# Kernel tuning notes

Hardware: AMD Instinct MI355X
Metric: run time of the kernel (lower is better)

Reference implementation:

```python
import jax, jax.numpy as jnp
import numpy as np

B, K, N, DIM, C_IN = 4, 2048, 4096, 3, 61
IN = DIM + C_IN        # 64, deepset input size
H1, H2 = 128, 128      # neighbor_xf hidden sizes
OUT = 64               # c_out // heads
HEADS = 4
EPS = 1e-5             # BatchNorm eps


def _lin(key, i, o):
    return jax.random.normal(key, (i, o), jnp.float32) * (1.0 / np.sqrt(i))


def setup_inputs() -> dict:
    key = jax.random.key(0)
    ks = jax.random.split(key, 12)
    return {
        "keys": jax.random.normal(ks[0], (B, K, DIM), jnp.float32),
        "points": jax.random.normal(ks[1], (B, N, DIM), jnp.float32),
        "feats": jax.random.normal(ks[2], (B, N, C_IN), jnp.float32),
        "nx_w1": _lin(ks[3], IN, H1), "nx_b1": jnp.zeros((H1,), jnp.float32),
        "nx_w2": _lin(ks[4], H1, H2), "nx_b2": jnp.zeros((H2,), jnp.float32),
        "nx_w3": _lin(ks[5], H2, OUT), "nx_b3": jnp.zeros((OUT,), jnp.float32),
        "sx_w1": _lin(ks[6], IN, IN), "sx_b1": jnp.zeros((IN,), jnp.float32),
        "sx_w2": _lin(ks[7], IN, IN), "sx_b2": jnp.zeros((IN,), jnp.float32),
        "sx_w3": _lin(ks[8], IN, IN), "sx_b3": jnp.zeros((IN,), jnp.float32),
        "att_w": _lin(ks[9], 2 * IN, HEADS * IN),
        "att_b": jnp.zeros((HEADS * IN,), jnp.float32),
        "att_q": jax.random.normal(ks[10], (HEADS, IN), jnp.float32) * 0.1,
        "bn_gamma": jnp.ones((IN,), jnp.float32),
        "bn_beta": jnp.zeros((IN,), jnp.float32),
        "neighbors": 32,
    }


def _mlp3(x, w1, b1, w2, b2, w3, b3):
    # per-element deepset MLP: Linear-ReLU-Linear-ReLU-Linear
    h = jax.nn.relu(x @ w1 + b1)
    h = jax.nn.relu(h @ w2 + b2)
    return h @ w3 + b3


def _forward(keys, points, feats, nx_w1, nx_b1, nx_w2, nx_b2, nx_w3, nx_b3,
             sx_w1, sx_b1, sx_w2, sx_b2, sx_w3, sx_b3,
             att_w, att_b, att_q, bn_gamma, bn_beta, neighbors):
    b = keys.shape[0]
    # Euclidean dist_fn: dist_vec [B,K,N,dim], dist [B,K,N], all points valid
    rel = points[:, None, :, :] - keys[:, :, None, :]
    dist = jnp.sqrt(jnp.sum(rel * rel, axis=-1))
    _, idx = jax.lax.top_k(-dist, neighbors)                   # [B,K,k] nearest
    nrel = jnp.take_along_axis(rel, idx[..., None], axis=2)    # [B,K,k,dim]
    bidx = jnp.arange(b)[:, None, None]
    nfeat = feats[bidx, idx]                                   # [B,K,k,c_in]
    comb = jnp.concatenate([nrel, nfeat], axis=-1)             # [B,K,k,in]
    lat = _mlp3(comb, nx_w1, nx_b1, nx_w2, nx_b2, nx_w3, nx_b3)  # [B,K,k,out]
    # BatchNorm1d (training-mode batch stats) over flattened [B*K*k, in]
    flat = comb.reshape(-1, comb.shape[-1])
    mean = jnp.mean(flat, axis=0)
    var = jnp.var(flat, axis=0)
    norm = (comb - mean) * jax.lax.rsqrt(var + EPS) * bn_gamma + bn_beta
    # SelfAttention: deepset sum-pooled context + per-neighbor softmax weights
    set_feat = jnp.sum(_mlp3(norm, sx_w1, sx_b1, sx_w2, sx_b2, sx_w3, sx_b3), axis=2)
    comb_feat = jnp.concatenate(
        [norm, jnp.broadcast_to(set_feat[:, :, None, :], norm.shape)], axis=-1)
    heads = (comb_feat @ att_w + att_b).reshape(comb_feat.shape[:3] + (HEADS, -1))
    e = jnp.sum(heads * att_q, axis=-1)                        # [B,K,k,H]
    w = jax.nn.softmax(e, axis=-2)                             # softmax over neighbor axis
    out = jnp.einsum('bkno,bknh->bkoh', lat, w)                # weighted reduce over k
    return out.reshape(out.shape[:2] + (-1,))                  # [B,K,out*H]


def reference(keys, points, feats, nx_w1, nx_b1, nx_w2, nx_b2, nx_w3, nx_b3,
              sx_w1, sx_b1, sx_w2, sx_b2, sx_w3, sx_b3,
              att_w, att_b, att_q, bn_gamma, bn_beta, neighbors):
    return _forward(keys, points, feats, nx_w1, nx_b1, nx_w2, nx_b2, nx_w3, nx_b3,
                    sx_w1, sx_b1, sx_w2, sx_b2, sx_w3, sx_b3,
                    att_w, att_b, att_q, bn_gamma, bn_beta, neighbors)
```

## Files before the change

### kernel.cpp

```cpp
#include <hip/hip_runtime.h>
#include <math.h>

#define BATCH 4
#define KQ    2048
#define NPTS  4096
#define CIN   61
#define KNN   32
#define ROWS  (BATCH*KQ*KNN)

#define OFF_IDX  0
#define OFF_ACC  524288
#define OFF_ATTA 557056
#define OFF_W1F  558080
#define OFF_W2F  574464
#define OFF_W3F  607232

typedef __attribute__((ext_vector_type(8)))  short bfrag;
typedef __attribute__((ext_vector_type(4)))  unsigned ufrag;
typedef __attribute__((ext_vector_type(16))) float cfrag;

__device__ __forceinline__ unsigned short bf16_rne(float x) {
  unsigned u = __float_as_uint(x);
  unsigned r = u + 0x7fffu + ((u >> 16) & 1u);
  return (unsigned short)(r >> 16);
}
__device__ __forceinline__ float4 ld4u(const float* p) {
  float4 r; __builtin_memcpy(&r, p, 16); return r;
}
__device__ __forceinline__ unsigned cvtpk(float lo, float hi) {
  unsigned r;
  asm("v_cvt_pk_bf16_f32 %0, %1, %2" : "=v"(r) : "v"(lo), "v"(hi));
  return r;
}
__device__ __forceinline__ float up_lo(unsigned pk) { return __uint_as_float(pk << 16); }
__device__ __forceinline__ float up_hi(unsigned pk) { return __uint_as_float(pk & 0xffff0000u); }

__device__ __forceinline__ cfrag zero16() {
  cfrag z;
#pragma unroll
  for (int i = 0; i < 16; ++i) z[i] = 0.f;
  return z;
}
__device__ __forceinline__ cfrag mfma_bu(bfrag a, ufrag b, cfrag c) {
  return __builtin_amdgcn_mfma_f32_32x32x16_bf16(a, __builtin_bit_cast(bfrag, b), c, 0, 0, 0);
}
__device__ __forceinline__ cfrag mfma_ub(ufrag a, bfrag b, cfrag c) {
  return __builtin_amdgcn_mfma_f32_32x32x16_bf16(__builtin_bit_cast(bfrag, a), b, c, 0, 0, 0);
}
__device__ __forceinline__ cfrag mfma_uu(ufrag a, ufrag b, cfrag c) {
  return __builtin_amdgcn_mfma_f32_32x32x16_bf16(__builtin_bit_cast(bfrag, a), __builtin_bit_cast(bfrag, b), c, 0, 0, 0);
}

#define NCAND 128

template<int NS>
__device__ __forceinline__ void select_emit(
    const unsigned* __restrict__ VAL, const unsigned short* __restrict__ IDXL,
    int mcount, unsigned hib, unsigned lob, int lane,
    const float* __restrict__ Pb, float kx, float ky, float kz,
    unsigned short* __restrict__ dst, int* __restrict__ SEL,
    float* __restrict__ accs) {
  const unsigned long long lmask = (1ull << lane) - 1ull;
  unsigned e[NS];
#pragma unroll
  for (int s = 0; s < NS; ++s) {
    int ei = s*64 + lane;
    e[s] = (ei < mcount) ? VAL[ei] : 0xffffffffu;
  }
  unsigned lo2 = lob, hi2 = hib;
  while (lo2 < hi2) {
    unsigned mid = lo2 + ((hi2 - lo2) >> 1);
    int c = 0;
#pragma unroll
    for (int s = 0; s < NS; ++s) c += (int)__popcll(__ballot(e[s] <= mid));
    if (c == KNN) { hi2 = mid; break; }
    if (c > KNN) hi2 = mid; else lo2 = mid + 1;
  }
  const unsigned T = hi2;
  float r0=0.f,r1=0.f,r2=0.f,r3=0.f,r4=0.f,r5=0.f;
  int base2 = 0;
#pragma unroll
  for (int s = 0; s < NS; ++s) {
    bool p = (e[s] <= T);
    unsigned long long m = __ballot(p);
    if (p) {
      int pos = base2 + (int)__popcll(m & lmask);
      if (pos < KNN) {
        int n = (int)IDXL[s*64 + lane];
        SEL[pos] = n;
        dst[pos] = (unsigned short)n;
        float dx = Pb[n*3+0]-kx, dy = Pb[n*3+1]-ky, dz = Pb[n*3+2]-kz;
        r0 += dx; r1 += dy; r2 += dz;
        r3 += dx*dx; r4 += dy*dy; r5 += dz*dz;
      }
    }
    base2 += (int)__popcll(m);
  }
#pragma unroll
  for (int off = 32; off > 0; off >>= 1) {
    r0 += __shfl_down(r0, off); r1 += __shfl_down(r1, off);
    r2 += __shfl_down(r2, off); r3 += __shfl_down(r3, off);
    r4 += __shfl_down(r4, off); r5 += __shfl_down(r5, off);
  }
  if (lane == 0) {
    atomicAdd(&accs[0], r0); atomicAdd(&accs[1], r1); atomicAdd(&accs[2], r2);
    atomicAdd(&accs[64], r3); atomicAdd(&accs[65], r4); atomicAdd(&accs[66], r5);
  }
}

__global__ __launch_bounds__(256, 4) void topk_kernel(
    const float* __restrict__ keys, const float* __restrict__ points,
    const float* __restrict__ feats,
    const float* __restrict__ w1, const float* __restrict__ w2,
    const float* __restrict__ w3,
    const float* __restrict__ att_w, const float* __restrict__ att_q,
    unsigned short* __restrict__ idx_out, float* __restrict__ acc,
    short* __restrict__ w1f, short* __restrict__ w2f, short* __restrict__ w3f,
    float* __restrict__ attA) {
  __shared__ unsigned VAL[4][NCAND];
  __shared__ unsigned short IDXL[4][NCAND];
  __shared__ int SEL[4][KNN];
  __shared__ float FRED[64*33];
  __shared__ float FQ[64*33];
  const int tid = threadIdx.x;
  const int lane = tid & 63, wid = tid >> 6;
  const int g0 = blockIdx.x * 4;
  const int b = g0 >> 11;
  const int gq = __builtin_amdgcn_readfirstlane(g0 + wid);
  const float kx = keys[(size_t)gq*3+0];
  const float ky = keys[(size_t)gq*3+1];
  const float kz = keys[(size_t)gq*3+2];
  const float* __restrict__ Pb = points + (size_t)b * NPTS * 3;

  unsigned u[64];
  unsigned lmin = 0xffffffffu;
#pragma unroll
  for (int jb = 0; jb < 8; ++jb) {
    float4 t[8];
#pragma unroll
    for (int q = 0; q < 8; ++q) {
      const int idx = (jb*8 + q)*64 + lane;
      if (jb == 7 && q == 7) {
        float4 tt = ld4u(Pb + (size_t)idx*3 - 1);
        t[q].x = tt.y; t[q].y = tt.z; t[q].z = tt.w; t[q].w = 0.f;
      } else {
        t[q] = ld4u(Pb + (size_t)idx*3);
      }
    }
#pragma unroll
    for (int q = 0; q < 8; ++q) {
      float dx = t[q].x - kx, dy = t[q].y - ky, dz = t[q].z - kz;
      unsigned d = __float_as_uint(dx*dx + dy*dy + dz*dz);
      u[jb*8 + q] = d;
      lmin = min(lmin, d);
    }
  }

  unsigned wlo = lmin, whi = lmin;
#pragma unroll
  for (int off = 1; off < 64; off <<= 1) {
    unsigned a0 = (unsigned)__shfl_xor((int)wlo, off);
    unsigned a1 = (unsigned)__shfl_xor((int)whi, off);
    wlo = min(wlo, a0); whi = max(whi, a1);
  }
  unsigned hib;
  {
    unsigned lo = wlo, hi = whi;
    while (lo < hi) {
      unsigned mid = lo + ((hi - lo) >> 1);
      int c = (int)__popcll(__ballot(lmin <= mid));
      if (c == KNN) { hi = mid; break; }
      if (c > KNN) hi = mid; else lo = mid + 1;
    }
    hib = hi;
  }

  int cnt = 0;
#pragma unroll
  for (int j = 0; j < 64; ++j) cnt += (u[j] <= hib) ? 1 : 0;
  int inc = cnt;
#pragma unroll
  for (int off = 1; off < 64; off <<= 1) {
    int t = __shfl_up(inc, off);
    if (lane >= off) inc += t;
  }
  const int mtot = __shfl(inc, 63);
  {
    int p = inc - cnt;
#pragma unroll
    for (int j = 0; j < 64; ++j) {
      if (u[j] <= hib) {
        if (p < NCAND) {
          VAL[wid][p] = u[j];
          IDXL[wid][p] = (unsigned short)(j*64 + lane);
        }
        ++p;
      }
    }
  }
  const int mcount = min(mtot, NCAND);

  float* accs = &acc[(blockIdx.x & 63)*128];
  if (mcount <= 64)
    select_emit<1>(VAL[wid], IDXL[wid], mcount, hib, wlo, lane, Pb,
                   kx, ky, kz, idx_out + (size_t)gq*KNN, SEL[wid], accs);
  else
    select_emit<2>(VAL[wid], IDXL[wid], mcount, hib, wlo, lane, Pb,
                   kx, ky, kz, idx_out + (size_t)gq*KNN, SEL[wid], accs);
  __syncthreads();

  {
    const int row = tid >> 3, chunk = tid & 7;
    const int nA = SEL[0][row], nB = SEL[1][row];
    const int nC = SEL[2][row], nD = SEL[3][row];
    const float* frA = feats + ((size_t)b*NPTS + nA)*CIN;
    const float* frB = feats + ((size_t)b*NPTS + nB)*CIN;
    const float* frC = feats + ((size_t)b*NPTS + nC)*CIN;
    const float* frD = feats + ((size_t)b*NPTS + nD)*CIN;
    float fs[8] = {0,0,0,0,0,0,0,0}, fq[8] = {0,0,0,0,0,0,0,0};
    if (chunk < 7) {
      const float* fr[4] = {frA, frB, frC, frD};
#pragma unroll
      for (int qq = 0; qq < 4; ++qq) {
        float4 a0 = ld4u(fr[qq] + chunk*8), a1 = ld4u(fr[qq] + chunk*8 + 4);
        fs[0]+=a0.x; fq[0]+=a0.x*a0.x; fs[1]+=a0.y; fq[1]+=a0.y*a0.y;
        fs[2]+=a0.z; fq[2]+=a0.z*a0.z; fs[3]+=a0.w; fq[3]+=a0.w*a0.w;
        fs[4]+=a1.x; fq[4]+=a1.x*a1.x; fs[5]+=a1.y; fq[5]+=a1.y*a1.y;
        fs[6]+=a1.z; fq[6]+=a1.z*a1.z; fs[7]+=a1.w; fq[7]+=a1.w*a1.w;
      }
    } else {
#pragma unroll
      for (int i = 0; i < 5; ++i) {
        float va = frA[56+i], vb = frB[56+i], vc = frC[56+i], vd = frD[56+i];
        fs[i] = va + vb + vc + vd;
        fq[i] = va*va + vb*vb + vc*vc + vd*vd;
      }
    }
#pragma unroll
    for (int i = 0; i < 8; ++i) {
      FRED[(chunk*8 + i)*33 + row] = fs[i];
      FQ  [(chunk*8 + i)*33 + row] = fq[i];
    }
  }
  __syncthreads();
  if (tid < 64) {
    float s = 0.f, q2 = 0.f;
#pragma unroll
    for (int r = 0; r < 32; ++r) {
      s  += FRED[tid*33 + r];
      q2 += FQ[tid*33 + r];
    }
    if (tid < CIN) {
      atomicAdd(&accs[3 + tid], s);
      atomicAdd(&accs[64 + 3 + tid], q2);
    }
  }

  if (blockIdx.x < 128) {
    const int t = blockIdx.x * 256 + tid;
    if (t < 8192) {
      int j = t & 7, ln = (t >> 3) & 63, tk = t >> 9;
      int kc = tk & 3, tile = tk >> 2;
      int nh = tile*32 + (ln & 31), k = kc*16 + (ln >> 5)*8 + j;
      w1f[t] = (short)bf16_rne(w1[k*128 + nh]);
    } else if (t < 24576) {
      int t2 = t - 8192;
      int j = t2 & 7, ln = (t2 >> 3) & 63, tk = t2 >> 9;
      int kc = tk & 7, tile = tk >> 3;
      int nh = tile*32 + (ln & 31);
      int k = 32*(kc>>1) + 16*(kc&1) + 4*(ln>>5) + (j&3) + 8*(j>>2);
      w2f[t2] = (short)bf16_rne(w2[k*128 + nh]);
    } else {
      int t3 = t - 24576;
      int j = t3 & 7, ln = (t3 >> 3) & 63, tk = t3 >> 9;
      int kc = tk & 7, tile = tk >> 3;
      int nh = tile*32 + (ln & 31);
      int k = 32*(kc>>1) + 16*(kc&1) + 4*(ln>>5) + (j&3) + 8*(j>>2);
      w3f[t3] = (short)bf16_rne(w3[k*64 + nh]);
    }
  } else if (blockIdx.x == 128) {
    const int t = tid, c = t >> 2, hh = t & 3;
    float s = 0.f;
    for (int d = 0; d < 64; ++d) s += att_w[c*256 + hh*64 + d] * att_q[hh*64 + d];
    attA[c*4 + hh] = s;
  }
}

#define L_W1F 0
#define L_W2F 16384
#define L_W3F 49152
#define L_SH  65536
#define L_SL  69632
#define L_B1  73728
#define L_B2  74240
#define L_B3  74752
#define L_WSC 75008
#define L_SC  79104
#define L_TOT 79360

__global__ __launch_bounds__(512, 4) void main_kernel(
    const float* __restrict__ keys, const float* __restrict__ points,
    const float* __restrict__ feats, const unsigned short* __restrict__ idxg,
    const short* __restrict__ w1f, const short* __restrict__ w2f,
    const short* __restrict__ w3f,
    const float* __restrict__ b1, const float* __restrict__ b2,
    const float* __restrict__ b3,
    const float* __restrict__ attAg, const float* __restrict__ accg,
    const float* __restrict__ gammav, float* __restrict__ out) {
  __shared__ __align__(16) char smem[L_TOT];
  const int tid = threadIdx.x;
  const int bid = blockIdx.x;
  const int wid = tid >> 6, lane = tid & 63;
  const int col = lane & 31, h = lane >> 5;

  float* WS = (float*)(smem + L_WSC) + wid*128;
  const short* SW1 = (const short*)(smem + L_W1F);
  const short* SW2 = (const short*)(smem + L_W2F);
  const short* SW3 = (const short*)(smem + L_W3F);
  const float* SB1 = (const float*)(smem + L_B1);
  const float* SB2 = (const float*)(smem + L_B2);

  auto gather_pack = [&](int g, int n, ufrag* ahi, ufrag* alo) {
    const int b = g >> 11;
    const float* frow = feats + ((size_t)b*NPTS + n)*CIN;
    float v[4][8];
    if (h == 0) {
      const float* Pb = points + (size_t)b*NPTS*3;
      v[0][0] = Pb[n*3+0] - keys[(size_t)g*3+0];
      v[0][1] = Pb[n*3+1] - keys[(size_t)g*3+1];
      v[0][2] = Pb[n*3+2] - keys[(size_t)g*3+2];
      float4 t0 = ld4u(frow);
      v[0][3]=t0.x; v[0][4]=t0.y; v[0][5]=t0.z; v[0][6]=t0.w;
      v[0][7] = frow[4];
    } else {
      float4 a0 = ld4u(frow+5), a1 = ld4u(frow+9);
      v[0][0]=a0.x; v[0][1]=a0.y; v[0][2]=a0.z; v[0][3]=a0.w;
      v[0][4]=a1.x; v[0][5]=a1.y; v[0][6]=a1.z; v[0][7]=a1.w;
    }
#pragma unroll
    for (int kc = 1; kc < 4; ++kc) {
      const int f0 = kc*16 + 8*h - 3;
      float4 a0 = ld4u(frow+f0), a1 = ld4u(frow+f0+4);
      v[kc][0]=a0.x; v[kc][1]=a0.y; v[kc][2]=a0.z; v[kc][3]=a0.w;
      v[kc][4]=a1.x; v[kc][5]=a1.y; v[kc][6]=a1.z; v[kc][7]=a1.w;
    }
#pragma unroll
    for (int kc = 0; kc < 4; ++kc)
#pragma unroll
      for (int p = 0; p < 4; ++p) {
        unsigned pk = cvtpk(v[kc][2*p], v[kc][2*p+1]);
        ahi[kc][p] = pk;
        alo[kc][p] = cvtpk(v[kc][2*p] - up_lo(pk), v[kc][2*p+1] - up_hi(pk));
      }
  };

  auto chain = [&](int g, const ufrag* ahi, const ufrag* alo) {
    cfrag Ef = zero16();
#pragma unroll
    for (int kc = 0; kc < 4; ++kc) {
      bfrag sh = *(const bfrag*)((const short*)(smem + L_SH) + (kc*64 + lane)*8);
      bfrag sl = *(const bfrag*)((const short*)(smem + L_SL) + (kc*64 + lane)*8);
      Ef = mfma_ub(ahi[kc], sh, Ef);
      Ef = mfma_ub(alo[kc], sh, Ef);
      Ef = mfma_ub(ahi[kc], sl, Ef);
    }

    float mx = Ef[0];
#pragma unroll
    for (int i = 1; i < 16; ++i) mx = fmaxf(mx, Ef[i]);
    mx = fmaxf(mx, __shfl_xor(mx, 32));
    float wsm[16], ssum = 0.f;
#pragma unroll
    for (int i = 0; i < 16; ++i) { wsm[i] = __expf(Ef[i] - mx); ssum += wsm[i]; }
    ssum += __shfl_xor(ssum, 32);
    const float invs = 1.f / ssum;
#pragma unroll
    for (int i = 0; i < 16; ++i) wsm[i] *= invs;

    if (col < 4) {
#pragma unroll
      for (int i = 0; i < 8; ++i) {
        const int c0 = (2*i & 3) + 8*(i >> 1);
        const int nA = c0 + 4*h;
        WS[nA*4 + col]     = wsm[2*i];
        WS[nA*4 + 4 + col] = wsm[2*i+1];
      }
    }
    const int hdc = col & 3;
    ufrag whi[2], wlo[2];
#pragma unroll
    for (int bb = 0; bb < 2; ++bb)
#pragma unroll
      for (int p = 0; p < 4; ++p) {
        const int c0 = (2*p & 3) + 8*(p >> 1);
        const int n0 = 16*bb + 4*h + c0;
        float r0 = WS[n0*4 + hdc], r1 = WS[n0*4 + 4 + hdc];
        unsigned pk = cvtpk(r0, r1);
        whi[bb][p] = pk;
        wlo[bb][p] = cvtpk(r0 - up_lo(pk), r1 - up_hi(pk));
      }

    ufrag a2[8];
#pragma unroll
    for (int t = 0; t < 4; ++t) {
      cfrag acc = zero16();
#pragma unroll
      for (int kc = 0; kc < 4; ++kc) {
        bfrag wf = *(const bfrag*)(SW1 + ((t*4 + kc)*64 + lane)*8);
        acc = mfma_bu(wf, ahi[kc], acc);
      }
#pragma unroll
      for (int i = 0; i < 8; ++i) {
        const int c0 = (2*i & 3) + 8*(i >> 1);
        float2 bb2 = *(const float2*)(SB1 + t*32 + c0 + 4*h);
        float x0 = fmaxf(acc[2*i]   + bb2.x, 0.f);
        float x1 = fmaxf(acc[2*i+1] + bb2.y, 0.f);
        a2[2*t + (i>>2)][i&3] = cvtpk(x0, x1);
      }
    }

    ufrag a3[8];
#pragma unroll
    for (int t = 0; t < 4; ++t) {
      cfrag acc = zero16();
#pragma unroll
      for (int kc = 0; kc < 8; ++kc) {
        bfrag wf = *(const bfrag*)(SW2 + ((t*8 + kc)*64 + lane)*8);
        acc = mfma_bu(wf, a2[kc], acc);
      }
#pragma unroll
      for (int i = 0; i < 8; ++i) {
        const int c0 = (2*i & 3) + 8*(i >> 1);
        float2 bb2 = *(const float2*)(SB2 + t*32 + c0 + 4*h);
        float x0 = fmaxf(acc[2*i]   + bb2.x, 0.f);
        float x1 = fmaxf(acc[2*i+1] + bb2.y, 0.f);
        a3[2*t + (i>>2)][i&3] = cvtpk(x0, x1);
      }
    }

#pragma unroll
    for (int t = 0; t < 2; ++t) {
      cfrag acc = zero16();
#pragma unroll
      for (int kc = 0; kc < 8; ++kc) {
        bfrag wf = *(const bfrag*)(SW3 + ((t*8 + kc)*64 + lane)*8);
        acc = mfma_ub(a3[kc], wf, acc);
      }
      const float bz = ((const float*)(smem + L_B3))[t*32 + col];
#pragma unroll
      for (int i = 0; i < 16; ++i) acc[i] += bz;
      ufrag lh[2], ll[2];
#pragma unroll
      for (int i = 0; i < 8; ++i) {
        unsigned pk = cvtpk(acc[2*i], acc[2*i+1]);
        lh[i>>2][i&3] = pk;
        ll[i>>2][i&3] = cvtpk(acc[2*i] - up_lo(pk), acc[2*i+1] - up_hi(pk));
      }
      cfrag og = zero16();
#pragma unroll
      for (int bb = 0; bb < 2; ++bb) og = mfma_uu(lh[bb], whi[bb], og);
#pragma unroll
      for (int bb = 0; bb < 2; ++bb) og = mfma_uu(ll[bb], whi[bb], og);
#pragma unroll
      for (int bb = 0; bb < 2; ++bb) og = mfma_uu(lh[bb], wlo[bb], og);
      if (col < 4) {
        float* op = out + (size_t)g*256 + t*128 + col;
#pragma unroll
        for (int i = 0; i < 16; ++i) {
          const int orow = (i&3) + 8*(i>>2) + 4*h;
          op[orow*4] = og[i];
        }
      }
    }
  };

  const int g0q = bid*8 + wid;
  const int g1q = g0q + 4096;
  const int n0 = (int)idxg[(size_t)g0q*KNN + col];
  const int n1 = (int)idxg[(size_t)g1q*KNN + col];
  ufrag ahi0[4], alo0[4];
  gather_pack(g0q, n0, ahi0, alo0);

  {
    const uint4* src = (const uint4*)w1f;
    uint4* dst = (uint4*)smem;
#pragma unroll
    for (int r = 0; r < 8; ++r) dst[r*512 + tid] = src[r*512 + tid];
    if (tid < 128) ((float*)(smem + L_B1))[tid] = b1[tid];
    else if (tid < 256) ((float*)(smem + L_B2))[tid-128] = b2[tid-128];
    else if (tid < 320) ((float*)(smem + L_B3))[tid-256] = b3[tid-256];
    float* TMP = (float*)(smem + L_WSC);
    {
      int c = tid & 63, p = tid >> 6;
      float s = 0.f, s2 = 0.f;
      for (int k = p; k < 64; k += 8) {
        s += accg[k*128 + c]; s2 += accg[k*128 + 64 + c];
      }
      TMP[p*128 + c] = s; TMP[p*128 + 64 + c] = s2;
    }
    __syncthreads();
    float* SCp = (float*)(smem + L_SC);
    if (tid < 64) {
      float s = 0.f, s2 = 0.f;
#pragma unroll
      for (int p = 0; p < 8; ++p) { s += TMP[p*128 + tid]; s2 += TMP[p*128 + 64 + tid]; }
      const float invR = 1.f / (float)ROWS;
      float mean = s * invR;
      float var = s2 * invR - mean * mean;
      SCp[tid] = gammav[tid] * rsqrtf(var + 1e-5f);
    }
    __syncthreads();
    {
      const int s = tid >> 8;
      const int kc = (tid >> 6) & 3;
      const int ln = tid & 63;
      const int hd = ln & 31;
      short* dstf = (short*)(smem + (s ? L_SL : L_SH)) + (kc*64 + ln)*8;
#pragma unroll
      for (int j = 0; j < 8; ++j) {
        const int ch = kc*16 + (ln>>5)*8 + j;
        float val = (hd < 4) ? attAg[ch*4 + hd] * SCp[ch] : 0.f;
        unsigned hb = bf16_rne(val);
        if (s) {
          float lo = val - __uint_as_float(hb << 16);
          dstf[j] = (short)bf16_rne(lo);
        } else {
          dstf[j] = (short)hb;
        }
      }
    }
    __syncthreads();
  }

  chain(g0q, ahi0, alo0);

  ufrag ahi1[4], alo1[4];
  gather_pack(g1q, n1, ahi1, alo1);
  chain(g1q, ahi1, alo1);
}

extern "C" void kernel_launch(void* const* d_in, const int* in_sizes, int n_in,
                              void* d_out, int out_size, void* d_ws, size_t ws_size,
                              hipStream_t stream) {
  const float* keys   = (const float*)d_in[0];
  const float* points = (const float*)d_in[1];
  const float* feats  = (const float*)d_in[2];
  const float* nx_w1  = (const float*)d_in[3];
  const float* nx_b1  = (const float*)d_in[4];
  const float* nx_w2  = (const float*)d_in[5];
  const float* nx_b2  = (const float*)d_in[6];
  const float* nx_w3  = (const float*)d_in[7];
  const float* nx_b3  = (const float*)d_in[8];
  const float* att_w  = (const float*)d_in[15];
  const float* att_q  = (const float*)d_in[17];
  const float* gamma  = (const float*)d_in[18];
  float* out = (float*)d_out;

  char* ws = (char*)d_ws;
  unsigned short* idxp = (unsigned short*)(ws + OFF_IDX);
  float* acc  = (float*)(ws + OFF_ACC);
  float* attA = (float*)(ws + OFF_ATTA);
  short* w1f  = (short*)(ws + OFF_W1F);
  short* w2f  = (short*)(ws + OFF_W2F);
  short* w3f  = (short*)(ws + OFF_W3F);

  hipMemsetAsync(acc, 0, 32768, stream);
  topk_kernel<<<2048, 256, 0, stream>>>(keys, points, feats,
      nx_w1, nx_w2, nx_w3, att_w, att_q, idxp, acc, w1f, w2f, w3f, attA);
  main_kernel<<<512, 512, 0, stream>>>(keys, points, feats, idxp,
      w1f, w2f, w3f, nx_b1, nx_b2, nx_b3, attA, acc, gamma, out);
}
```

Before: 161.1 us.

## Recompute distances instead of holding 64 per lane; raise occupancy bound

Drops the 64-register per-lane distance array. After the threshold search, the kernel reloads the points and recomputes their distances, then appends candidates into LDS through per-wave shared atomic counters instead of a prefix-scan compaction. The launch bound goes from 4 to 6 waves per SIMD to use the freed registers. In exchange it loads the points twice, adds LDS atomics, and stores candidates in nondeterministic order. There is also no barrier between initialising WCNT and the first atomic on it, which relies on wave-local ordering.

```diff
diff --git a/kernel.cpp b/kernel.cpp
--- a/kernel.cpp
+++ b/kernel.cpp
@@ -108,7 +108,7 @@
   }
 }
 
-__global__ __launch_bounds__(256, 4) void topk_kernel(
+__global__ __launch_bounds__(256, 6) void topk_kernel(
     const float* __restrict__ keys, const float* __restrict__ points,
     const float* __restrict__ feats,
     const float* __restrict__ w1, const float* __restrict__ w2,
@@ -120,6 +120,7 @@
   __shared__ unsigned VAL[4][NCAND];
   __shared__ unsigned short IDXL[4][NCAND];
   __shared__ int SEL[4][KNN];
+  __shared__ int WCNT[4];
   __shared__ float FRED[64*33];
   __shared__ float FQ[64*33];
   const int tid = threadIdx.x;
@@ -132,7 +133,8 @@
   const float kz = keys[(size_t)gq*3+2];
   const float* __restrict__ Pb = points + (size_t)b * NPTS * 3;
 
-  unsigned u[64];
+  if (lane == 0) WCNT[wid] = 0;
+
   unsigned lmin = 0xffffffffu;
 #pragma unroll
   for (int jb = 0; jb < 8; ++jb) {
@@ -150,9 +152,7 @@
 #pragma unroll
     for (int q = 0; q < 8; ++q) {
       float dx = t[q].x - kx, dy = t[q].y - ky, dz = t[q].z - kz;
-      unsigned d = __float_as_uint(dx*dx + dy*dy + dz*dz);
-      u[jb*8 + q] = d;
-      lmin = min(lmin, d);
+      lmin = min(lmin, __float_as_uint(dx*dx + dy*dy + dz*dz));
     }
   }
 
@@ -175,30 +175,33 @@
     hib = hi;
   }
 
-  int cnt = 0;
-#pragma unroll
-  for (int j = 0; j < 64; ++j) cnt += (u[j] <= hib) ? 1 : 0;
-  int inc = cnt;
-#pragma unroll
-  for (int off = 1; off < 64; off <<= 1) {
-    int t = __shfl_up(inc, off);
-    if (lane >= off) inc += t;
-  }
-  const int mtot = __shfl(inc, 63);
-  {
-    int p = inc - cnt;
-#pragma unroll
-    for (int j = 0; j < 64; ++j) {
-      if (u[j] <= hib) {
-        if (p < NCAND) {
-          VAL[wid][p] = u[j];
-          IDXL[wid][p] = (unsigned short)(j*64 + lane);
+#pragma unroll
+  for (int jb = 0; jb < 8; ++jb) {
+    float4 t[8];
+#pragma unroll
+    for (int q = 0; q < 8; ++q) {
+      const int idx = (jb*8 + q)*64 + lane;
+      if (jb == 7 && q == 7) {
+        float4 tt = ld4u(Pb + (size_t)idx*3 - 1);
+        t[q].x = tt.y; t[q].y = tt.z; t[q].z = tt.w; t[q].w = 0.f;
+      } else {
+        t[q] = ld4u(Pb + (size_t)idx*3);
+      }
+    }
+#pragma unroll
+    for (int q = 0; q < 8; ++q) {
+      float dx = t[q].x - kx, dy = t[q].y - ky, dz = t[q].z - kz;
+      unsigned d = __float_as_uint(dx*dx + dy*dy + dz*dz);
+      if (d <= hib) {
+        int pos = atomicAdd(&WCNT[wid], 1);
+        if (pos < NCAND) {
+          VAL[wid][pos] = d;
+          IDXL[wid][pos] = (unsigned short)((jb*8 + q)*64 + lane);
         }
-        ++p;
-      }
-    }
-  }
-  const int mcount = min(mtot, NCAND);
+      }
+    }
+  }
+  const int mcount = min(WCNT[wid], NCAND);
 
   float* accs = &acc[(blockIdx.x & 63)*128];
   if (mcount <= 64)
```

New measurement: 278.7 us. +73.0%, slower.
